# Kernel optimization log

Hardware: AMD Instinct MI355X
Metric: run time of the kernel (lower is better)

Reference implementation:

```python
import jax, jax.numpy as jnp
import numpy as np

B, T, C = 2, 2048, 1024
H, HS, RD = 16, 64, 64
KV_R, Q_R = 256, 384


def _rope_tables(T, dim):
    # standard RoPE angle tables, shape [T, dim]
    half = dim // 2
    inv_freq = 1.0 / (10000.0 ** (np.arange(0, half, dtype=np.float32) / half))
    t = np.arange(T, dtype=np.float32)
    ang = np.outer(t, inv_freq)  # [T, half]
    ang = np.concatenate([ang, ang], axis=-1)  # [T, dim]
    return jnp.asarray(np.cos(ang)), jnp.asarray(np.sin(ang))


def setup_inputs() -> dict:
    key = jax.random.key(0)
    ks = jax.random.split(key, 8)
    cos, sin = _rope_tables(T, RD)
    s = lambda fan_in: 1.0 / np.sqrt(fan_in)
    return {
        "x": jax.random.normal(ks[0], (B, T, C), jnp.float32),
        "cos": cos,
        "sin": sin,
        "W_kv_down": jax.random.normal(ks[1], (C, KV_R), jnp.float32) * s(C),
        "W_kv_up": jax.random.normal(ks[2], (KV_R, H * HS), jnp.float32) * s(KV_R),
        "W_k_rope": jax.random.normal(ks[3], (KV_R, H * RD), jnp.float32) * s(KV_R),
        "W_q_down": jax.random.normal(ks[4], (C, Q_R), jnp.float32) * s(C),
        "W_q_up": jax.random.normal(ks[5], (Q_R, H * HS), jnp.float32) * s(Q_R),
        "W_q_rope": jax.random.normal(ks[6], (Q_R, H * RD), jnp.float32) * s(Q_R),
        "W_out": jax.random.normal(ks[7], (H * HS, C), jnp.float32) * s(H * HS),
    }


def _apply_rope(x, cos, sin):
    # x: [B,H,T,D]; cos/sin: [T,D] broadcast
    d = x.shape[-1]
    x1, x2 = x[..., : d // 2], x[..., d // 2 :]
    rotated = jnp.concatenate([-x2, x1], axis=-1)
    return x * cos + rotated * sin


def reference(x, cos, sin, W_kv_down, W_kv_up, W_k_rope, W_q_down, W_q_up, W_q_rope, W_out):
    Bx, Tx, Cx = x.shape
    to_heads = lambda z, d: jnp.swapaxes(z.reshape(Bx, Tx, H, d), 1, 2)  # [B,H,T,d]

    latent_kv = x @ W_kv_down                      # [B,T,KV_R]
    kv_up = latent_kv @ W_kv_up                    # [B,T,H*HS]
    v = to_heads(kv_up, HS)
    k_content = to_heads(kv_up, HS)                # same projection used for k and v
    k_rope = _apply_rope(to_heads(latent_kv @ W_k_rope, RD), cos[:Tx], sin[:Tx])

    latent_q = x @ W_q_down                        # [B,T,Q_R]
    q_content = to_heads(latent_q @ W_q_up, HS)
    q_rope = _apply_rope(to_heads(latent_q @ W_q_rope, RD), cos[:Tx], sin[:Tx])

    q = jnp.concatenate([q_content, q_rope], axis=-1)  # [B,H,T,HS+RD]
    k = jnp.concatenate([k_content, k_rope], axis=-1)

    att = jnp.einsum("bhqd,bhkd->bhqk", q, k) * (HS ** -0.5)
    causal = jnp.tril(jnp.ones((Tx, Tx), bool))
    att = jnp.where(causal, att, -jnp.inf)
    att = jax.nn.softmax(att, axis=-1)             # dropout is eval-mode identity
    y = jnp.einsum("bhqk,bhkd->bhqd", att, v)      # [B,H,T,HS]
    y = jnp.swapaxes(y, 1, 2).reshape(Bx, Tx, H * HS)
    return y @ W_out
```

## Files before the change

kernel.cpp:

```cpp
#include <hip/hip_runtime.h>
#include <stdint.h>

typedef unsigned short u16;
typedef __bf16 bf16x8 __attribute__((ext_vector_type(8)));
typedef float f32x4 __attribute__((ext_vector_type(4)));

#define B_ 2
#define T_ 2048

__device__ __forceinline__ u16 f2b(float f) {
  unsigned u = __float_as_uint(f);
  u += 0x7fffu + ((u >> 16) & 1u);
  return (u16)(u >> 16);
}
__device__ __forceinline__ float b2f(u16 v) {
  return __uint_as_float(((unsigned)v) << 16);
}
__device__ __forceinline__ unsigned cvt_pk(float lo, float hi) {
  unsigned r;
  asm("v_cvt_pk_bf16_f32 %0, %1, %2" : "=v"(r) : "v"(lo), "v"(hi));
  return r;
}
__device__ __forceinline__ float ex2(float x) {
  float r;
  asm("v_exp_f32 %0, %1" : "=v"(r) : "v"(x));
  return r;
}

using gu32 = __attribute__((address_space(1))) const unsigned int;
using lu32 = __attribute__((address_space(3))) unsigned int;
__device__ __forceinline__ void gl_lds16(const u16* g, u16* l) {
  __builtin_amdgcn_global_load_lds((gu32*)g, (lu32*)l, 16, 0, 0);
}

__global__ __launch_bounds__(256) void conv_x_kernel(const float* __restrict__ in,
                                                     u16* __restrict__ out) {
  int i = (blockIdx.x * 256 + threadIdx.x) * 4;
  float4 v = *reinterpret_cast<const float4*>(in + i);
  union { u16 h[4]; unsigned long long ll; } pk;
  pk.h[0] = f2b(v.x); pk.h[1] = f2b(v.y); pk.h[2] = f2b(v.z); pk.h[3] = f2b(v.w);
  *reinterpret_cast<unsigned long long*>(out + i) = pk.ll;
}

struct TJob { const float* src; u16* dst; int K, N, ldt, row_off, blk0; };
struct TJobs { TJob j[7]; };

__global__ __launch_bounds__(256) void transpose_all_kernel(TJobs jobs) {
  __shared__ float tile[32][33];
  int bid = blockIdx.x;
  int ji = 0;
  #pragma unroll
  for (int i = 6; i > 0; --i)
    if (bid >= jobs.j[i].blk0) { ji = i; break; }
  const TJob jb = jobs.j[ji];
  int local = bid - jb.blk0;
  int nb = jb.N >> 5;
  int n0 = (local % nb) * 32, k0 = (local / nb) * 32;
  int cx = threadIdx.x, ry = threadIdx.y;
  #pragma unroll
  for (int i = 0; i < 4; i++)
    tile[ry + i * 8][cx] = jb.src[(size_t)(k0 + ry + i * 8) * jb.N + n0 + cx];
  __syncthreads();
  #pragma unroll
  for (int i = 0; i < 4; i++)
    jb.dst[(size_t)(jb.row_off + n0 + ry + i * 8) * jb.ldt + k0 + cx] =
        f2b(tile[cx][ry + i * 8]);
}

__global__ __launch_bounds__(256) void gemm_bt(const u16* __restrict__ A, int lda,
                                               const u16* __restrict__ Bt, int ldb,
                                               void* __restrict__ Cout, int ldc,
                                               int K, int mode, u16* __restrict__ vt,
                                               const float* __restrict__ cosT,
                                               const float* __restrict__ sinT) {
  __shared__ u16 As[2][128 * 32];
  __shared__ u16 Bs[2][128 * 32];
  const int tid = threadIdx.x;
  const int wave = tid >> 6, lane = tid & 63;
  const int wr = wave >> 1, wc = wave & 1;
  const int l15 = lane & 15, l4 = lane >> 4;
  const int m0 = blockIdx.y * 128, n0 = blockIdx.x * 128;
  const int lr = lane >> 2;
  const int lc = (lane & 3) * 8;

  f32x4 acc[4][4];
  const f32x4 fzero = {0.f, 0.f, 0.f, 0.f};
  #pragma unroll
  for (int m = 0; m < 4; m++)
    #pragma unroll
    for (int n = 0; n < 4; n++)
      acc[m][n] = fzero;

  const u16* gA  = A  + (size_t)(m0 + wave * 32 + lr) * lda + lc;
  const u16* gA2 = gA + (size_t)16 * lda;
  const u16* gB  = Bt + (size_t)(n0 + wave * 32 + lr) * ldb + lc;
  const u16* gB2 = gB + (size_t)16 * ldb;

  auto stage = [&](int buf, int k0) {
    gl_lds16(gA + k0, &As[buf][(wave * 32) * 32]);
    gl_lds16(gA2 + k0, &As[buf][(wave * 32 + 16) * 32]);
    gl_lds16(gB + k0, &Bs[buf][(wave * 32) * 32]);
    gl_lds16(gB2 + k0, &Bs[buf][(wave * 32 + 16) * 32]);
  };

  stage(0, 0);
  __syncthreads();
  int buf = 0;
  for (int k0 = 0; k0 < K; k0 += 32) {
    if (k0 + 32 < K) stage(buf ^ 1, k0 + 32);
    bf16x8 af[4], bfr[4];
    #pragma unroll
    for (int m = 0; m < 4; m++)
      af[m] = *reinterpret_cast<const bf16x8*>(&As[buf][(wr * 64 + m * 16 + l15) * 32 + l4 * 8]);
    #pragma unroll
    for (int n = 0; n < 4; n++)
      bfr[n] = *reinterpret_cast<const bf16x8*>(&Bs[buf][(wc * 64 + n * 16 + l15) * 32 + l4 * 8]);
    #pragma unroll
    for (int m = 0; m < 4; m++)
      #pragma unroll
      for (int n = 0; n < 4; n++)
        acc[m][n] = __builtin_amdgcn_mfma_f32_16x16x32_bf16(af[m], bfr[n], acc[m][n], 0, 0, 0);
    __syncthreads();
    buf ^= 1;
  }

  const int row_base = m0 + wr * 64 + l4 * 4;
  const int col_base = n0 + wc * 64 + l15;

  if (mode == 1) {
    float* Cf = (float*)Cout;
    #pragma unroll
    for (int m = 0; m < 4; m++)
      #pragma unroll
      for (int n = 0; n < 4; n++)
        #pragma unroll
        for (int r = 0; r < 4; r++)
          Cf[(size_t)(row_base + m * 16 + r) * ldc + col_base + n * 16] = acc[m][n][r];
    return;
  }

  if (mode >= 2 && (n0 + wc * 64) >= 1024) {
    #pragma unroll
    for (int m = 0; m < 4; m++)
      #pragma unroll
      for (int r = 0; r < 4; r++) {
        int t = (row_base + m * 16 + r) & (T_ - 1);
        const float* cp = cosT + t * 64 + l15;
        const float* sp = sinT + t * 64 + l15;
        float c0 = cp[0], c16 = cp[16], c32 = cp[32], c48 = cp[48];
        float s0 = sp[0], s16 = sp[16], s32 = sp[32], s48 = sp[48];
        float x0 = acc[m][0][r], x1 = acc[m][1][r];
        float x2 = acc[m][2][r], x3 = acc[m][3][r];
        acc[m][0][r] = x0 * c0 - x2 * s0;
        acc[m][1][r] = x1 * c16 - x3 * s16;
        acc[m][2][r] = x2 * c32 + x0 * s32;
        acc[m][3][r] = x3 * c48 + x1 * s48;
      }
  }

  u16* Cb = (u16*)Cout;
  #pragma unroll
  for (int m = 0; m < 4; m++)
    #pragma unroll
    for (int n = 0; n < 4; n++)
      #pragma unroll
      for (int r = 0; r < 4; r++)
        Cb[(size_t)(row_base + m * 16 + r) * ldc + col_base + n * 16] = f2b(acc[m][n][r]);

  if (mode == 2) {
    #pragma unroll
    for (int m = 0; m < 4; m++)
      #pragma unroll
      for (int n = 0; n < 4; n++) {
        int col = col_base + n * 16;
        if (col < 1024) {
          int mm = row_base + m * 16;
          int bb = mm >> 11, tt = mm & 2047;
          uint2 pk2;
          pk2.x = cvt_pk(acc[m][n][0], acc[m][n][1]);
          pk2.y = cvt_pk(acc[m][n][2], acc[m][n][3]);
          *reinterpret_cast<uint2*>(&vt[(size_t)(bb * 1024 + col) * 2048 + tt]) = pk2;
        }
      }
  }
}

__global__ __launch_bounds__(512) void attn_kernel(const u16* __restrict__ qo,
                                                   const u16* __restrict__ kvo,
                                                   const u16* __restrict__ vtg,
                                                   u16* __restrict__ yb) {
  __shared__ u16 K_lds[2][64 * 128];
  __shared__ u16 V_lds[2][64 * 64];
  __shared__ u16 P_lds[8][16][72];
  const int tid = threadIdx.x;
  const int wave = tid >> 6, lane = tid & 63;
  const int l15 = lane & 15, l4 = lane >> 4;
  const int bid = blockIdx.x;
  const int bh = bid & 31;
  const int qi = 15 - (bid >> 5);
  const int b = bh >> 4, h = bh & 15;
  const int q0 = qi * 128;
  const int qrow = q0 + wave * 16 + l15;

  const u16* qb = qo + (size_t)(b * T_ + qrow) * 2048 + h * 64;
  bf16x8 qf[4];
  qf[0] = *reinterpret_cast<const bf16x8*>(qb + l4 * 8);
  qf[1] = *reinterpret_cast<const bf16x8*>(qb + 32 + l4 * 8);
  qf[2] = *reinterpret_cast<const bf16x8*>(qb + 1024 + l4 * 8);
  qf[3] = *reinterpret_cast<const bf16x8*>(qb + 1056 + l4 * 8);

  const u16* Kbase = kvo + (size_t)(b * T_) * 2048 + h * 64;
  const u16* Vbase = vtg + (size_t)(b * 1024 + h * 64) * 2048;

  const int krow_i = lane >> 4;
  const int kc2 = (lane & 15) * 16;
  const int vrow_i = lane >> 3;
  const int vc2 = (lane & 7) * 16;

  auto stage = [&](int buf, int kv0) {
    #pragma unroll
    for (int j = 0; j < 2; j++) {
      int row = wave * 8 + j * 4 + krow_i;
      int c2x = kc2 ^ ((row & 7) << 4);
      int cu = c2x >> 1;
      const u16* src = Kbase + (size_t)(kv0 + row) * 2048 + (cu < 64 ? cu : 960 + cu);
      gl_lds16(src, &K_lds[buf][(wave * 8 + j * 4) * 128]);
    }
    {
      int row = wave * 8 + vrow_i;
      int c2x = vc2 ^ ((row & 7) << 4);
      const u16* src = Vbase + (size_t)row * 2048 + kv0 + (c2x >> 1);
      gl_lds16(src, &V_lds[buf][(wave * 8) * 64]);
    }
  };

  const f32x4 fzero = {0.f, 0.f, 0.f, 0.f};
  f32x4 oT[4];
  #pragma unroll
  for (int f = 0; f < 4; f++) oT[f] = fzero;
  float m_run = -1e30f, l_run = 0.f;

  const float SCALE2 = 0.125f * 1.44269504f;
  const int nt = qi * 2 + 2;
  const int t_diag = qi * 2 + (wave >> 2);

  stage(0, 0);
  __syncthreads();
  int buf = 0;

  for (int t = 0; t < nt; t++) {
    const int kv0 = t * 64;
    if (t + 1 < nt) stage(buf ^ 1, kv0 + 64);

    if (t <= t_diag) {
      const char* Kb = (const char*)&K_lds[buf][0];
      const char* Vb = (const char*)&V_lds[buf][0];

      f32x4 sT[4];
      #pragma unroll
      for (int c = 0; c < 4; c++) sT[c] = fzero;
      #pragma unroll
      for (int c = 0; c < 4; c++) {
        const int krow = c * 16 + l15;
        const int kxm = (krow & 7) << 4;
        #pragma unroll
        for (int s = 0; s < 4; s++) {
          bf16x8 kf = *reinterpret_cast<const bf16x8*>(
              Kb + krow * 256 + ((s * 64 + l4 * 16) ^ kxm));
          sT[c] = __builtin_amdgcn_mfma_f32_16x16x32_bf16(kf, qf[s], sT[c], 0, 0, 0);
        }
      }

      const bool diag = (t == t_diag);
      float p[4][4];
      float mx = -1e30f;
      #pragma unroll
      for (int c = 0; c < 4; c++)
        #pragma unroll
        for (int r = 0; r < 4; r++) {
          float s = sT[c][r] * SCALE2;
          if (diag) {
            int kv = kv0 + c * 16 + l4 * 4 + r;
            if (kv > qrow) s = -1e30f;
          }
          p[c][r] = s;
          mx = fmaxf(mx, s);
        }
      mx = fmaxf(mx, __shfl_xor(mx, 16));
      mx = fmaxf(mx, __shfl_xor(mx, 32));
      if (__any(mx > m_run + 11.5f)) {
        float m_new = fmaxf(m_run, mx);
        float corr = ex2(m_run - m_new);
        l_run *= corr;
        #pragma unroll
        for (int f = 0; f < 4; f++) oT[f] *= corr;
        m_run = m_new;
      }
      float rsum = 0.f;
      #pragma unroll
      for (int c = 0; c < 4; c++)
        #pragma unroll
        for (int r = 0; r < 4; r++) {
          float pe = ex2(p[c][r] - m_run);
          p[c][r] = pe;
          rsum += pe;
        }
      rsum += __shfl_xor(rsum, 16);
      rsum += __shfl_xor(rsum, 32);
      l_run += rsum;

      #pragma unroll
      for (int c = 0; c < 4; c++) {
        uint2 pk2;
        pk2.x = cvt_pk(p[c][0], p[c][1]);
        pk2.y = cvt_pk(p[c][2], p[c][3]);
        *reinterpret_cast<uint2*>(&P_lds[wave][l15][c * 16 + l4 * 4]) = pk2;
      }
      bf16x8 pb0 = *reinterpret_cast<const bf16x8*>(&P_lds[wave][l15][l4 * 8]);
      bf16x8 pb1 = *reinterpret_cast<const bf16x8*>(&P_lds[wave][l15][32 + l4 * 8]);

      #pragma unroll
      for (int f = 0; f < 4; f++) {
        const int vrow = f * 16 + l15;
        const int vxm = (vrow & 7) << 4;
        bf16x8 v0 = *reinterpret_cast<const bf16x8*>(Vb + vrow * 128 + ((l4 * 16) ^ vxm));
        bf16x8 v1 = *reinterpret_cast<const bf16x8*>(Vb + vrow * 128 + ((64 + l4 * 16) ^ vxm));
        oT[f] = __builtin_amdgcn_mfma_f32_16x16x32_bf16(v0, pb0, oT[f], 0, 0, 0);
        oT[f] = __builtin_amdgcn_mfma_f32_16x16x32_bf16(v1, pb1, oT[f], 0, 0, 0);
      }
    }

    __syncthreads();
    buf ^= 1;
  }

  const float inv = 1.f / l_run;
  #pragma unroll
  for (int f = 0; f < 4; f++) {
    uint2 pk2;
    pk2.x = cvt_pk(oT[f][0] * inv, oT[f][1] * inv);
    pk2.y = cvt_pk(oT[f][2] * inv, oT[f][3] * inv);
    *reinterpret_cast<uint2*>(
        &yb[(size_t)(b * T_ + qrow) * 1024 + h * 64 + f * 16 + l4 * 4]) = pk2;
  }
}

extern "C" void kernel_launch(void* const* d_in, const int* in_sizes, int n_in,
                              void* d_out, int out_size, void* d_ws, size_t ws_size,
                              hipStream_t stream) {
  const float* x         = (const float*)d_in[0];
  const float* cosT      = (const float*)d_in[1];
  const float* sinT      = (const float*)d_in[2];
  const float* W_kv_down = (const float*)d_in[3];
  const float* W_kv_up   = (const float*)d_in[4];
  const float* W_k_rope  = (const float*)d_in[5];
  const float* W_q_down  = (const float*)d_in[6];
  const float* W_q_up    = (const float*)d_in[7];
  const float* W_q_rope  = (const float*)d_in[8];
  const float* W_out     = (const float*)d_in[9];
  float* out = (float*)d_out;
  char* ws = (char*)d_ws;

  u16* xb    = (u16*)(ws + 0);
  u16* lat   = (u16*)(ws + 8388608);
  u16* WdT   = (u16*)(ws + 13631488);
  u16* WkvT  = (u16*)(ws + 14942208);
  u16* WqT   = (u16*)(ws + 15990784);
  u16* WoutT = (u16*)(ws + 17563648);
  u16* kvo   = (u16*)(ws + 19660800);
  u16* qo    = (u16*)(ws + 36438016);
  u16* VT    = (u16*)(ws + 53215232);
  u16* yb    = (u16*)(ws + 0);

  conv_x_kernel<<<4096, 256, 0, stream>>>(x, xb);

  TJobs jobs;
  jobs.j[0] = {W_kv_down, WdT,   1024, 256,  1024, 0,    0};
  jobs.j[1] = {W_q_down,  WdT,   1024, 384,  1024, 256,  256};
  jobs.j[2] = {W_kv_up,   WkvT,  256,  1024, 256,  0,    640};
  jobs.j[3] = {W_k_rope,  WkvT,  256,  1024, 256,  1024, 896};
  jobs.j[4] = {W_q_up,    WqT,   384,  1024, 384,  0,    1152};
  jobs.j[5] = {W_q_rope,  WqT,   384,  1024, 384,  1024, 1536};
  jobs.j[6] = {W_out,     WoutT, 1024, 1024, 1024, 0,    1920};
  transpose_all_kernel<<<2944, dim3(32, 8), 0, stream>>>(jobs);

  gemm_bt<<<dim3(5, 32), 256, 0, stream>>>(xb, 1024, WdT, 1024, lat, 640, 1024, 0,
                                           nullptr, nullptr, nullptr);
  gemm_bt<<<dim3(16, 32), 256, 0, stream>>>(lat, 640, WkvT, 256, kvo, 2048, 256, 2,
                                            VT, cosT, sinT);
  gemm_bt<<<dim3(16, 32), 256, 0, stream>>>(lat + 256, 640, WqT, 384, qo, 2048, 384, 3,
                                            nullptr, cosT, sinT);

  attn_kernel<<<512, 512, 0, stream>>>(qo, kvo, VT, yb);

  gemm_bt<<<dim3(8, 32), 256, 0, stream>>>(yb, 1024, WoutT, 1024, out, 1024, 1024, 1,
                                           nullptr, nullptr, nullptr);
}
```

Measured before the change: 231.0 us.

## Merge prep and projection launches, use 8-wave GEMM blocks, single-barrier pipelines

Result: faster. 220.1 us (-4.7%).

```diff
diff --git a/kernel.cpp b/kernel.cpp
--- a/kernel.cpp
+++ b/kernel.cpp
@@ -33,21 +33,23 @@
   __builtin_amdgcn_global_load_lds((gu32*)g, (lu32*)l, 16, 0, 0);
 }
 
-__global__ __launch_bounds__(256) void conv_x_kernel(const float* __restrict__ in,
-                                                     u16* __restrict__ out) {
-  int i = (blockIdx.x * 256 + threadIdx.x) * 4;
-  float4 v = *reinterpret_cast<const float4*>(in + i);
-  union { u16 h[4]; unsigned long long ll; } pk;
-  pk.h[0] = f2b(v.x); pk.h[1] = f2b(v.y); pk.h[2] = f2b(v.z); pk.h[3] = f2b(v.w);
-  *reinterpret_cast<unsigned long long*>(out + i) = pk.ll;
-}
-
 struct TJob { const float* src; u16* dst; int K, N, ldt, row_off, blk0; };
 struct TJobs { TJob j[7]; };
 
-__global__ __launch_bounds__(256) void transpose_all_kernel(TJobs jobs) {
+__global__ __launch_bounds__(256) void prep_kernel(const float* __restrict__ x,
+                                                   u16* __restrict__ xb, TJobs jobs) {
+  int bid = blockIdx.x;
+  int tid = threadIdx.x;
+  if (bid < 4096) {
+    int i = (bid * 256 + tid) * 4;
+    float4 v = *reinterpret_cast<const float4*>(x + i);
+    union { u16 h[4]; unsigned long long ll; } pk;
+    pk.h[0] = f2b(v.x); pk.h[1] = f2b(v.y); pk.h[2] = f2b(v.z); pk.h[3] = f2b(v.w);
+    *reinterpret_cast<unsigned long long*>(xb + i) = pk.ll;
+    return;
+  }
+  bid -= 4096;
   __shared__ float tile[32][33];
-  int bid = blockIdx.x;
   int ji = 0;
   #pragma unroll
   for (int i = 6; i > 0; --i)
@@ -56,7 +58,7 @@
   int local = bid - jb.blk0;
   int nb = jb.N >> 5;
   int n0 = (local % nb) * 32, k0 = (local / nb) * 32;
-  int cx = threadIdx.x, ry = threadIdx.y;
+  int cx = tid & 31, ry = tid >> 5;
   #pragma unroll
   for (int i = 0; i < 4; i++)
     tile[ry + i * 8][cx] = jb.src[(size_t)(k0 + ry + i * 8) * jb.N + n0 + cx];
@@ -67,70 +69,72 @@
         f2b(tile[cx][ry + i * 8]);
 }
 
-__global__ __launch_bounds__(256) void gemm_bt(const u16* __restrict__ A, int lda,
-                                               const u16* __restrict__ Bt, int ldb,
-                                               void* __restrict__ Cout, int ldc,
-                                               int K, int mode, u16* __restrict__ vt,
-                                               const float* __restrict__ cosT,
-                                               const float* __restrict__ sinT) {
+struct GJob { const u16* A; const u16* Bt; void* C; int lda, ldb, ldc, K, mode; };
+
+__global__ __launch_bounds__(512) void gemm_bt8(GJob j0, GJob j1, int split,
+                                                u16* __restrict__ vt,
+                                                const float* __restrict__ cosT,
+                                                const float* __restrict__ sinT) {
   __shared__ u16 As[2][128 * 32];
   __shared__ u16 Bs[2][128 * 32];
+  const bool first = (int)blockIdx.x < split;
+  const GJob jb = first ? j0 : j1;
+  const int bx = blockIdx.x - (first ? 0 : split);
   const int tid = threadIdx.x;
   const int wave = tid >> 6, lane = tid & 63;
   const int wr = wave >> 1, wc = wave & 1;
   const int l15 = lane & 15, l4 = lane >> 4;
-  const int m0 = blockIdx.y * 128, n0 = blockIdx.x * 128;
+  const int m0 = blockIdx.y * 128, n0 = bx * 128;
   const int lr = lane >> 2;
   const int lc = (lane & 3) * 8;
 
-  f32x4 acc[4][4];
+  f32x4 acc[2][4];
   const f32x4 fzero = {0.f, 0.f, 0.f, 0.f};
   #pragma unroll
-  for (int m = 0; m < 4; m++)
+  for (int m = 0; m < 2; m++)
     #pragma unroll
     for (int n = 0; n < 4; n++)
       acc[m][n] = fzero;
 
-  const u16* gA  = A  + (size_t)(m0 + wave * 32 + lr) * lda + lc;
-  const u16* gA2 = gA + (size_t)16 * lda;
-  const u16* gB  = Bt + (size_t)(n0 + wave * 32 + lr) * ldb + lc;
-  const u16* gB2 = gB + (size_t)16 * ldb;
+  const u16* gA = jb.A  + (size_t)(m0 + wave * 16 + lr) * jb.lda + lc;
+  const u16* gB = jb.Bt + (size_t)(n0 + wave * 16 + lr) * jb.ldb + lc;
 
   auto stage = [&](int buf, int k0) {
-    gl_lds16(gA + k0, &As[buf][(wave * 32) * 32]);
-    gl_lds16(gA2 + k0, &As[buf][(wave * 32 + 16) * 32]);
-    gl_lds16(gB + k0, &Bs[buf][(wave * 32) * 32]);
-    gl_lds16(gB2 + k0, &Bs[buf][(wave * 32 + 16) * 32]);
+    gl_lds16(gA + k0, &As[buf][(wave * 16) * 32]);
+    gl_lds16(gB + k0, &Bs[buf][(wave * 16) * 32]);
   };
 
   stage(0, 0);
-  __syncthreads();
   int buf = 0;
+  const int K = jb.K;
   for (int k0 = 0; k0 < K; k0 += 32) {
+    asm volatile("s_waitcnt vmcnt(0)" ::: "memory");
+    __builtin_amdgcn_s_barrier();
     if (k0 + 32 < K) stage(buf ^ 1, k0 + 32);
-    bf16x8 af[4], bfr[4];
-    #pragma unroll
-    for (int m = 0; m < 4; m++)
-      af[m] = *reinterpret_cast<const bf16x8*>(&As[buf][(wr * 64 + m * 16 + l15) * 32 + l4 * 8]);
+    bf16x8 af[2], bfr[4];
+    #pragma unroll
+    for (int m = 0; m < 2; m++)
+      af[m] = *reinterpret_cast<const bf16x8*>(&As[buf][(wr * 32 + m * 16 + l15) * 32 + l4 * 8]);
     #pragma unroll
     for (int n = 0; n < 4; n++)
       bfr[n] = *reinterpret_cast<const bf16x8*>(&Bs[buf][(wc * 64 + n * 16 + l15) * 32 + l4 * 8]);
     #pragma unroll
-    for (int m = 0; m < 4; m++)
+    for (int m = 0; m < 2; m++)
       #pragma unroll
       for (int n = 0; n < 4; n++)
         acc[m][n] = __builtin_amdgcn_mfma_f32_16x16x32_bf16(af[m], bfr[n], acc[m][n], 0, 0, 0);
-    __syncthreads();
     buf ^= 1;
   }
 
-  const int row_base = m0 + wr * 64 + l4 * 4;
+  const int row_base = m0 + wr * 32 + l4 * 4;
   const int col_base = n0 + wc * 64 + l15;
+  const int mode = jb.mode;
+  const int ldc = jb.ldc;
 
   if (mode == 1) {
-    float* Cf = (float*)Cout;
-    #pragma unroll
-    for (int m = 0; m < 4; m++)
+    float* Cf = (float*)jb.C;
+    #pragma unroll
+    for (int m = 0; m < 2; m++)
       #pragma unroll
       for (int n = 0; n < 4; n++)
         #pragma unroll
@@ -141,7 +145,7 @@
 
   if (mode >= 2 && (n0 + wc * 64) >= 1024) {
     #pragma unroll
-    for (int m = 0; m < 4; m++)
+    for (int m = 0; m < 2; m++)
       #pragma unroll
       for (int r = 0; r < 4; r++) {
         int t = (row_base + m * 16 + r) & (T_ - 1);
@@ -158,9 +162,9 @@
       }
   }
 
-  u16* Cb = (u16*)Cout;
-  #pragma unroll
-  for (int m = 0; m < 4; m++)
+  u16* Cb = (u16*)jb.C;
+  #pragma unroll
+  for (int m = 0; m < 2; m++)
     #pragma unroll
     for (int n = 0; n < 4; n++)
       #pragma unroll
@@ -169,7 +173,7 @@
 
   if (mode == 2) {
     #pragma unroll
-    for (int m = 0; m < 4; m++)
+    for (int m = 0; m < 2; m++)
       #pragma unroll
       for (int n = 0; n < 4; n++) {
         int col = col_base + n * 16;
@@ -245,11 +249,12 @@
   const int t_diag = qi * 2 + (wave >> 2);
 
   stage(0, 0);
-  __syncthreads();
   int buf = 0;
 
   for (int t = 0; t < nt; t++) {
     const int kv0 = t * 64;
+    asm volatile("s_waitcnt vmcnt(0)" ::: "memory");
+    __builtin_amdgcn_s_barrier();
     if (t + 1 < nt) stage(buf ^ 1, kv0 + 64);
 
     if (t <= t_diag) {
@@ -330,7 +335,6 @@
       }
     }
 
-    __syncthreads();
     buf ^= 1;
   }
 
@@ -372,8 +376,6 @@
   u16* VT    = (u16*)(ws + 53215232);
   u16* yb    = (u16*)(ws + 0);
 
-  conv_x_kernel<<<4096, 256, 0, stream>>>(x, xb);
-
   TJobs jobs;
   jobs.j[0] = {W_kv_down, WdT,   1024, 256,  1024, 0,    0};
   jobs.j[1] = {W_q_down,  WdT,   1024, 384,  1024, 256,  256};
@@ -382,17 +384,17 @@
   jobs.j[4] = {W_q_up,    WqT,   384,  1024, 384,  0,    1152};
   jobs.j[5] = {W_q_rope,  WqT,   384,  1024, 384,  1024, 1536};
   jobs.j[6] = {W_out,     WoutT, 1024, 1024, 1024, 0,    1920};
-  transpose_all_kernel<<<2944, dim3(32, 8), 0, stream>>>(jobs);
-
-  gemm_bt<<<dim3(5, 32), 256, 0, stream>>>(xb, 1024, WdT, 1024, lat, 640, 1024, 0,
-                                           nullptr, nullptr, nullptr);
-  gemm_bt<<<dim3(16, 32), 256, 0, stream>>>(lat, 640, WkvT, 256, kvo, 2048, 256, 2,
-                                            VT, cosT, sinT);
-  gemm_bt<<<dim3(16, 32), 256, 0, stream>>>(lat + 256, 640, WqT, 384, qo, 2048, 384, 3,
-                                            nullptr, cosT, sinT);
+  prep_kernel<<<7040, 256, 0, stream>>>(x, xb, jobs);
+
+  GJob g1 = {xb, WdT, lat, 1024, 1024, 640, 1024, 0};
+  gemm_bt8<<<dim3(5, 32), 512, 0, stream>>>(g1, g1, 5, nullptr, nullptr, nullptr);
+
+  GJob g2 = {lat,       WkvT, kvo, 640, 256, 2048, 256, 2};
+  GJob g3 = {lat + 256, WqT,  qo,  640, 384, 2048, 384, 3};
+  gemm_bt8<<<dim3(32, 32), 512, 0, stream>>>(g2, g3, 16, VT, cosT, sinT);
 
   attn_kernel<<<512, 512, 0, stream>>>(qo, kvo, VT, yb);
 
-  gemm_bt<<<dim3(8, 32), 256, 0, stream>>>(yb, 1024, WoutT, 1024, out, 1024, 1024, 1,
-                                           nullptr, nullptr, nullptr);
-}
+  GJob g4 = {yb, WoutT, out, 1024, 1024, 1024, 1024, 1};
+  gemm_bt8<<<dim3(8, 32), 512, 0, stream>>>(g4, g4, 8, nullptr, nullptr, nullptr);
+}
```
